# Performance work log

Hardware: AMD Instinct MI355X
Metric: run time of the kernel (lower is better)

## Reference

```python
import jax, jax.numpy as jnp
import numpy as np

DIM = 384
NUM_HEADS = 8


def setup_inputs() -> dict:
    key = jax.random.key(0)
    k1, k2, k3, k4 = jax.random.split(key, 4)
    B, N, D = 8, 16384, DIM
    x = jax.random.normal(k1, (B, N, D), dtype=jnp.float32)
    # nn.Linear(dim, 3*dim, bias=False): weight [3D, D]; store transposed [D, 3D]
    W_qkv = jax.random.normal(k2, (D, 3 * D), dtype=jnp.float32) * (1.0 / np.sqrt(D))
    W_proj = jax.random.normal(k3, (D, D), dtype=jnp.float32) * (1.0 / np.sqrt(D))
    b_proj = jax.random.normal(k4, (D,), dtype=jnp.float32) * 0.01
    return {"x": x, "W_qkv": W_qkv, "W_proj": W_proj, "b_proj": b_proj}


def reference(x, W_qkv, W_proj, b_proj):
    B, N, D = x.shape
    H = NUM_HEADS
    C = D // H
    # qkv: [B, N, 3, H, C] -> split; layout matches '(qkv H C)' packing
    qkv = (x @ W_qkv).reshape(B, N, 3, H, C)
    qkv = jnp.transpose(qkv, (2, 0, 3, 1, 4))  # [3, B, H, N, C]
    q = jax.nn.softmax(qkv[0], axis=-1)        # softmax over channel dim C
    k = jax.nn.softmax(qkv[1], axis=2)         # softmax over token dim N (== B H C N softmax last)
    v = qkv[2]
    # context = k^T @ v : [B, H, C, C] — tiny, avoids NxN scores
    context = jnp.einsum('bhnc,bhnd->bhcd', k, v)
    out = jnp.einsum('bhnc,bhcd->bhnd', q, context)  # [B, H, N, C]
    out = jnp.transpose(out, (0, 2, 1, 3)).reshape(B, N, D)  # 'B H N C -> B N (H C)'
    return out @ W_proj + b_proj
```

## Files before the change

kernel.cpp:

```cpp
#include <hip/hip_runtime.h>
#include <math.h>

#define B_ 8
#define N_ 16384
#define D_ 384
#define TD_ 1152
#define M_ (B_*N_)
#define CTX_ELEMS (B_*8*48*48)
#define Z_ELEMS   (B_*8*48)

typedef __attribute__((ext_vector_type(8))) short short8;
typedef __attribute__((ext_vector_type(4))) float f32x4;
typedef __attribute__((ext_vector_type(4))) unsigned short us4;
typedef __attribute__((ext_vector_type(8))) unsigned short us8;

__device__ __forceinline__ unsigned short f2bf(float f){
    union { float f; unsigned u; } v; v.f = f;
    unsigned r = v.u + 0x7FFFu + ((v.u >> 16) & 1u);
    return (unsigned short)(r >> 16);
}

#define MFMA(a,b,c) __builtin_amdgcn_mfma_f32_16x16x32_bf16((a),(b),(c),0,0,0)

__global__ void kP(const float* __restrict__ Wqkv, const float* __restrict__ Wp,
                   unsigned short* __restrict__ WqkvT, unsigned short* __restrict__ WpT)
{
    __shared__ float t[32][33];
    int bi = blockIdx.x;
    const float* src; unsigned short* dst; int ldS, c0, d0;
    if (bi < 432) { src = Wqkv; dst = WqkvT; ldS = 1152; c0 = (bi % 36) * 32; d0 = (bi / 36) * 32; }
    else { bi -= 432; src = Wp; dst = WpT; ldS = 384; c0 = (bi % 12) * 32; d0 = (bi / 12) * 32; }
    const int cx = threadIdx.x & 31, ry = threadIdx.x >> 5;
#pragma unroll
    for (int k = 0; k < 4; ++k) {
        int r = ry + k * 8;
        t[r][cx] = src[(size_t)(d0 + r) * ldS + c0 + cx];
    }
    __syncthreads();
#pragma unroll
    for (int k = 0; k < 4; ++k) {
        int r = ry + k * 8;
        dst[(size_t)(c0 + r) * 384 + d0 + cx] = f2bf(t[cx][r]);
    }
}

__global__ __launch_bounds__(512, 2) void kA(const float* __restrict__ x,
        const unsigned short* __restrict__ WqkvT,
        float* __restrict__ ctx, float* __restrict__ Z)
{
    __shared__ __align__(16) unsigned short xs[64 * 392];
    __shared__ __align__(16) unsigned short kv[8 * 96 * 64];

    const int tid = threadIdx.x;
    const int w   = tid >> 6;
    const int l   = tid & 63;
    const int q   = l >> 4;
    const int c16 = l & 15;
    const int blk = blockIdx.x;
    const int b   = blk >> 5;
    const int tbase = (blk & 31) * 8;
    unsigned short* kvw = kv + w * (96 * 64);

    f32x4 ctxacc[3][3];
    float zp[3] = {0.f, 0.f, 0.f};
#pragma unroll
    for (int i = 0; i < 3; ++i)
#pragma unroll
        for (int j = 0; j < 3; ++j) ctxacc[i][j] = (f32x4){0.f, 0.f, 0.f, 0.f};

    const int st = tid >> 3, sq = tid & 7;

    for (int g = 0; g < 8; ++g) {
        const size_t tok0 = (size_t)b * 16384 + (size_t)(tbase + g) * 64;
        __syncthreads();
        {
            const float* xg = x + (tok0 + st) * 384 + sq * 4;
            unsigned short* xw = xs + st * 392 + sq * 4;
#pragma unroll
            for (int i = 0; i < 12; ++i) {
                float4 v = *(const float4*)(xg + i * 32);
                us4 o; o.x = f2bf(v.x); o.y = f2bf(v.y); o.z = f2bf(v.z); o.w = f2bf(v.w);
                *(us4*)(xw + i * 32) = o;
            }
        }
        __syncthreads();

        f32x4 kva[4][6];
#pragma unroll
        for (int mt = 0; mt < 4; ++mt)
#pragma unroll
            for (int j = 0; j < 6; ++j) kva[mt][j] = (f32x4){0.f, 0.f, 0.f, 0.f};

#pragma unroll
        for (int ks = 0; ks < 12; ++ks) {
            short8 a[4];
#pragma unroll
            for (int mt = 0; mt < 4; ++mt)
                a[mt] = *(const short8*)(xs + (mt * 16 + c16) * 392 + ks * 32 + q * 8);
#pragma unroll
            for (int j = 0; j < 6; ++j) {
                const int colrow = (j < 3) ? (384 + w * 48 + j * 16 + c16)
                                           : (768 + w * 48 + (j - 3) * 16 + c16);
                short8 bf = *(const short8*)(WqkvT + (size_t)colrow * 384 + ks * 32 + q * 8);
#pragma unroll
                for (int mt = 0; mt < 4; ++mt)
                    kva[mt][j] = MFMA(a[mt], bf, kva[mt][j]);
            }
        }

#pragma unroll
        for (int mt = 0; mt < 4; ++mt) {
            const int chunk = 2 * mt + (q >> 1);
            const int tin = (q & 1) * 4;
#pragma unroll
            for (int j = 0; j < 6; ++j) {
                f32x4 vv = kva[mt][j];
                us4 o;
                int row;
                if (j < 3) {
                    row = j * 16 + c16;
                    float e0 = __expf(vv.x), e1 = __expf(vv.y), e2 = __expf(vv.z), e3 = __expf(vv.w);
                    zp[j] += (e0 + e1) + (e2 + e3);
                    o.x = f2bf(e0); o.y = f2bf(e1); o.z = f2bf(e2); o.w = f2bf(e3);
                } else {
                    row = 48 + (j - 3) * 16 + c16;
                    o.x = f2bf(vv.x); o.y = f2bf(vv.y); o.z = f2bf(vv.z); o.w = f2bf(vv.w);
                }
                *(us4*)(kvw + row * 64 + ((chunk ^ (row & 7)) << 3) + tin) = o;
            }
        }
        __syncthreads();

#pragma unroll
        for (int kt = 0; kt < 2; ++kt) {
            short8 af[3], bf2[3];
#pragma unroll
            for (int i = 0; i < 3; ++i) {
                const int ra = i * 16 + c16;
                af[i]  = *(const short8*)(kvw + ra * 64 + (((kt * 4 + q) ^ (ra & 7)) << 3));
                const int rb = 48 + i * 16 + c16;
                bf2[i] = *(const short8*)(kvw + rb * 64 + (((kt * 4 + q) ^ (rb & 7)) << 3));
            }
#pragma unroll
            for (int ct = 0; ct < 3; ++ct)
#pragma unroll
                for (int dt = 0; dt < 3; ++dt)
                    ctxacc[ct][dt] = MFMA(af[ct], bf2[dt], ctxacc[ct][dt]);
        }
    }

#pragma unroll
    for (int j = 0; j < 3; ++j) {
        float v = zp[j];
        v += __shfl_xor(v, 16);
        v += __shfl_xor(v, 32);
        if (l < 16) atomicAdd(&Z[(b * 8 + w) * 48 + j * 16 + c16], v);
    }
#pragma unroll
    for (int ct = 0; ct < 3; ++ct)
#pragma unroll
        for (int dt = 0; dt < 3; ++dt)
#pragma unroll
            for (int r = 0; r < 4; ++r) {
                const int c = ct * 16 + q * 4 + r;
                const int d = dt * 16 + c16;
                atomicAdd(&ctx[((size_t)(b * 8 + w) * 48 + c) * 48 + d], ctxacc[ct][dt][r]);
            }
}

__global__ void kB(const float* __restrict__ ctx, const float* __restrict__ Z,
                   unsigned short* __restrict__ ctxT)
{
    const int e = blockIdx.x * 256 + threadIdx.x;
    const int bh = e / 3072;
    const int r = e % 3072;
    const int d = r >> 6;
    const int c = r & 63;
    float v = 0.f;
    if (c < 48) v = ctx[((size_t)bh * 48 + c) * 48 + d] / Z[bh * 48 + c];
    ctxT[e] = f2bf(v);
}

__global__ __launch_bounds__(256, 2) void kC(const float* __restrict__ x,
        const unsigned short* __restrict__ WqkvT,
        const unsigned short* __restrict__ ctxT,
        const unsigned short* __restrict__ WpT,
        const float* __restrict__ bp, float* __restrict__ out)
{
    __shared__ __align__(16) unsigned short xs[32 * 392];
    __shared__ __align__(16) unsigned short qs[32 * 520];

    const int tid = threadIdx.x;
    const int w   = tid >> 6;
    const int l   = tid & 63;
    const int q   = l >> 4;
    const int c16 = l & 15;
    const int blk = blockIdx.x;
    const size_t tok0 = (size_t)blk * 32;
    const int b = blk >> 9;

    {
        const int st = tid >> 3, sq = tid & 7;
        const float* xg = x + (tok0 + st) * 384 + sq * 4;
        unsigned short* xw = xs + st * 392 + sq * 4;
#pragma unroll
        for (int i = 0; i < 12; ++i) {
            float4 v = *(const float4*)(xg + i * 32);
            us4 o; o.x = f2bf(v.x); o.y = f2bf(v.y); o.z = f2bf(v.z); o.w = f2bf(v.w);
            *(us4*)(xw + i * 32) = o;
        }
    }
    __syncthreads();

    f32x4 acc[2][6];
#pragma unroll
    for (int mt = 0; mt < 2; ++mt)
#pragma unroll
        for (int j = 0; j < 6; ++j) acc[mt][j] = (f32x4){0.f, 0.f, 0.f, 0.f};

#pragma unroll
    for (int ks = 0; ks < 12; ++ks) {
        short8 a0 = *(const short8*)(xs + (c16) * 392 + ks * 32 + q * 8);
        short8 a1 = *(const short8*)(xs + (16 + c16) * 392 + ks * 32 + q * 8);
#pragma unroll
        for (int j = 0; j < 6; ++j) {
            const int nt = w * 6 + j;
            short8 bf = *(const short8*)(WqkvT + (size_t)(nt * 16 + c16) * 384 + ks * 32 + q * 8);
            acc[0][j] = MFMA(a0, bf, acc[0][j]);
            acc[1][j] = MFMA(a1, bf, acc[1][j]);
        }
    }
    __syncthreads();

#pragma unroll
    for (int hh = 0; hh < 2; ++hh) {
        const int h = 2 * w + hh;
        f32x4 e[2][3];
#pragma unroll
        for (int mt = 0; mt < 2; ++mt)
#pragma unroll
            for (int jj = 0; jj < 3; ++jj) {
                f32x4 vv = acc[mt][hh * 3 + jj];
                e[mt][jj].x = __expf(vv.x); e[mt][jj].y = __expf(vv.y);
                e[mt][jj].z = __expf(vv.z); e[mt][jj].w = __expf(vv.w);
            }
#pragma unroll
        for (int mt = 0; mt < 2; ++mt)
#pragma unroll
            for (int r = 0; r < 4; ++r) {
                float s = e[mt][0][r] + e[mt][1][r] + e[mt][2][r];
                s += __shfl_xor(s, 1); s += __shfl_xor(s, 2);
                s += __shfl_xor(s, 4); s += __shfl_xor(s, 8);
                const float inv = 1.0f / s;
                e[mt][0][r] *= inv; e[mt][1][r] *= inv; e[mt][2][r] *= inv;
            }
#pragma unroll
        for (int mt = 0; mt < 2; ++mt)
#pragma unroll
            for (int jj = 0; jj < 3; ++jj) {
                const int c = jj * 16 + c16;
#pragma unroll
                for (int r = 0; r < 4; ++r) {
                    const int t = mt * 16 + q * 4 + r;
                    qs[t * 520 + h * 64 + c] = f2bf(e[mt][jj][r]);
                }
            }
    }
    {
        const int t = l & 31, hp = l >> 5;
        const int h = 2 * w + hp;
        us8 z8 = {0, 0, 0, 0, 0, 0, 0, 0};
        *(us8*)(qs + t * 520 + h * 64 + 48) = z8;
    }
    __syncthreads();

#pragma unroll
    for (int hh = 0; hh < 2; ++hh) {
        const int h = 2 * w + hh;
        f32x4 y[2][3];
#pragma unroll
        for (int mt = 0; mt < 2; ++mt)
#pragma unroll
            for (int dt = 0; dt < 3; ++dt) y[mt][dt] = (f32x4){0.f, 0.f, 0.f, 0.f};
#pragma unroll
        for (int ks = 0; ks < 2; ++ks) {
            short8 a0 = *(const short8*)(qs + (c16) * 520 + h * 64 + ks * 32 + q * 8);
            short8 a1 = *(const short8*)(qs + (16 + c16) * 520 + h * 64 + ks * 32 + q * 8);
#pragma unroll
            for (int dt = 0; dt < 3; ++dt) {
                short8 bf = *(const short8*)(ctxT + ((size_t)(b * 8 + h) * 48 + dt * 16 + c16) * 64 + ks * 32 + q * 8);
                y[0][dt] = MFMA(a0, bf, y[0][dt]);
                y[1][dt] = MFMA(a1, bf, y[1][dt]);
            }
        }
#pragma unroll
        for (int mt = 0; mt < 2; ++mt)
#pragma unroll
            for (int dt = 0; dt < 3; ++dt) {
                const int dcol = h * 48 + dt * 16 + c16;
#pragma unroll
                for (int r = 0; r < 4; ++r) {
                    const int t = mt * 16 + q * 4 + r;
                    xs[t * 392 + dcol] = f2bf(y[mt][dt][r]);
                }
            }
    }
    __syncthreads();

    f32x4 po[2][6];
#pragma unroll
    for (int mt = 0; mt < 2; ++mt)
#pragma unroll
        for (int j = 0; j < 6; ++j) po[mt][j] = (f32x4){0.f, 0.f, 0.f, 0.f};

#pragma unroll
    for (int ks = 0; ks < 12; ++ks) {
        short8 a0 = *(const short8*)(xs + (c16) * 392 + ks * 32 + q * 8);
        short8 a1 = *(const short8*)(xs + (16 + c16) * 392 + ks * 32 + q * 8);
#pragma unroll
        for (int j = 0; j < 6; ++j) {
            const int nt = w * 6 + j;
            short8 bf = *(const short8*)(WpT + (size_t)(nt * 16 + c16) * 384 + ks * 32 + q * 8);
            po[0][j] = MFMA(a0, bf, po[0][j]);
            po[1][j] = MFMA(a1, bf, po[1][j]);
        }
    }

#pragma unroll
    for (int j = 0; j < 6; ++j) {
        const int col = (w * 6 + j) * 16 + c16;
        const float bv = bp[col];
#pragma unroll
        for (int mt = 0; mt < 2; ++mt)
#pragma unroll
            for (int r = 0; r < 4; ++r) {
                const int t = mt * 16 + q * 4 + r;
                out[(tok0 + t) * 384 + col] = po[mt][j][r] + bv;
            }
    }
}

extern "C" void kernel_launch(void* const* d_in, const int* in_sizes, int n_in,
                              void* d_out, int out_size, void* d_ws, size_t ws_size,
                              hipStream_t stream)
{
    (void)in_sizes; (void)n_in; (void)out_size; (void)ws_size;
    const float* x    = (const float*)d_in[0];
    const float* Wqkv = (const float*)d_in[1];
    const float* Wp   = (const float*)d_in[2];
    const float* bp   = (const float*)d_in[3];
    float* out = (float*)d_out;

    char* p = (char*)d_ws;
    float* ctx = (float*)p;                 p += CTX_ELEMS * 4;
    float* Z   = (float*)p;                 p += Z_ELEMS * 4;
    unsigned short* WqkvT = (unsigned short*)p;  p += TD_ * D_ * 2;
    unsigned short* WpT   = (unsigned short*)p;  p += D_ * D_ * 2;
    unsigned short* ctxT  = (unsigned short*)p;

    hipMemsetAsync(d_ws, 0, (CTX_ELEMS + Z_ELEMS) * sizeof(float), stream);
    kP<<<dim3(576), dim3(256), 0, stream>>>(Wqkv, Wp, WqkvT, WpT);
    kA<<<dim3(256), dim3(512), 0, stream>>>(x, WqkvT, ctx, Z);
    kB<<<dim3(768), dim3(256), 0, stream>>>(ctx, Z, ctxT);
    kC<<<dim3(4096), dim3(256), 0, stream>>>(x, WqkvT, ctxT, WpT, bp, out);
}
```

Baseline: 824.8 us.

## Shrink kA token tile to 32 and double grid; per-wave q buffer in kC

kA now processes 32-token tiles instead of 64, computing the K and V halves sequentially to cut accumulator registers and LDS, with launch bounds raised to 4 blocks and the grid doubled to 512 blocks. This is meant to raise occupancy and spread the work over more CUs, at the cost of more global atomics on ctx and Z and more repeated weight loads. kC gives each wave its own small q staging buffer so the q@ctx product follows softmax directly, without a block-wide barrier. Its launch bounds are raised to 3 blocks per CU.

```diff
diff --git a/kernel.cpp b/kernel.cpp
--- a/kernel.cpp
+++ b/kernel.cpp
@@ -44,12 +44,12 @@
     }
 }
 
-__global__ __launch_bounds__(512, 2) void kA(const float* __restrict__ x,
+__global__ __launch_bounds__(512, 4) void kA(const float* __restrict__ x,
         const unsigned short* __restrict__ WqkvT,
         float* __restrict__ ctx, float* __restrict__ Z)
 {
-    __shared__ __align__(16) unsigned short xs[64 * 392];
-    __shared__ __align__(16) unsigned short kv[8 * 96 * 64];
+    __shared__ __align__(16) unsigned short xs[32 * 392];
+    __shared__ __align__(16) unsigned short kv[8 * 96 * 32];
 
     const int tid = threadIdx.x;
     const int w   = tid >> 6;
@@ -57,9 +57,9 @@
     const int q   = l >> 4;
     const int c16 = l & 15;
     const int blk = blockIdx.x;
-    const int b   = blk >> 5;
-    const int tbase = (blk & 31) * 8;
-    unsigned short* kvw = kv + w * (96 * 64);
+    const int b   = blk >> 6;
+    const int tile0 = (blk & 63) * 8;
+    unsigned short* kvw = kv + w * (96 * 32);
 
     f32x4 ctxacc[3][3];
     float zp[3] = {0.f, 0.f, 0.f};
@@ -68,85 +68,78 @@
 #pragma unroll
         for (int j = 0; j < 3; ++j) ctxacc[i][j] = (f32x4){0.f, 0.f, 0.f, 0.f};
 
-    const int st = tid >> 3, sq = tid & 7;
+    const int st = tid >> 4, sq = tid & 15;
 
     for (int g = 0; g < 8; ++g) {
-        const size_t tok0 = (size_t)b * 16384 + (size_t)(tbase + g) * 64;
+        const size_t tok0 = (size_t)b * 16384 + (size_t)(tile0 + g) * 32;
         __syncthreads();
         {
             const float* xg = x + (tok0 + st) * 384 + sq * 4;
             unsigned short* xw = xs + st * 392 + sq * 4;
 #pragma unroll
-            for (int i = 0; i < 12; ++i) {
-                float4 v = *(const float4*)(xg + i * 32);
+            for (int i = 0; i < 6; ++i) {
+                float4 v = *(const float4*)(xg + i * 64);
                 us4 o; o.x = f2bf(v.x); o.y = f2bf(v.y); o.z = f2bf(v.z); o.w = f2bf(v.w);
-                *(us4*)(xw + i * 32) = o;
+                *(us4*)(xw + i * 64) = o;
             }
         }
         __syncthreads();
 
-        f32x4 kva[4][6];
-#pragma unroll
-        for (int mt = 0; mt < 4; ++mt)
-#pragma unroll
-            for (int j = 0; j < 6; ++j) kva[mt][j] = (f32x4){0.f, 0.f, 0.f, 0.f};
-
-#pragma unroll
-        for (int ks = 0; ks < 12; ++ks) {
-            short8 a[4];
-#pragma unroll
-            for (int mt = 0; mt < 4; ++mt)
-                a[mt] = *(const short8*)(xs + (mt * 16 + c16) * 392 + ks * 32 + q * 8);
-#pragma unroll
-            for (int j = 0; j < 6; ++j) {
-                const int colrow = (j < 3) ? (384 + w * 48 + j * 16 + c16)
-                                           : (768 + w * 48 + (j - 3) * 16 + c16);
-                short8 bf = *(const short8*)(WqkvT + (size_t)colrow * 384 + ks * 32 + q * 8);
-#pragma unroll
-                for (int mt = 0; mt < 4; ++mt)
-                    kva[mt][j] = MFMA(a[mt], bf, kva[mt][j]);
-            }
-        }
-
-#pragma unroll
-        for (int mt = 0; mt < 4; ++mt) {
-            const int chunk = 2 * mt + (q >> 1);
-            const int tin = (q & 1) * 4;
-#pragma unroll
-            for (int j = 0; j < 6; ++j) {
-                f32x4 vv = kva[mt][j];
-                us4 o;
-                int row;
-                if (j < 3) {
-                    row = j * 16 + c16;
-                    float e0 = __expf(vv.x), e1 = __expf(vv.y), e2 = __expf(vv.z), e3 = __expf(vv.w);
-                    zp[j] += (e0 + e1) + (e2 + e3);
-                    o.x = f2bf(e0); o.y = f2bf(e1); o.z = f2bf(e2); o.w = f2bf(e3);
-                } else {
-                    row = 48 + (j - 3) * 16 + c16;
-                    o.x = f2bf(vv.x); o.y = f2bf(vv.y); o.z = f2bf(vv.z); o.w = f2bf(vv.w);
+#pragma unroll
+        for (int half = 0; half < 2; ++half) {
+            f32x4 acc2[2][3];
+#pragma unroll
+            for (int mt = 0; mt < 2; ++mt)
+#pragma unroll
+                for (int j = 0; j < 3; ++j) acc2[mt][j] = (f32x4){0.f, 0.f, 0.f, 0.f};
+
+#pragma unroll
+            for (int ks = 0; ks < 12; ++ks) {
+                short8 a0 = *(const short8*)(xs + (c16) * 392 + ks * 32 + q * 8);
+                short8 a1 = *(const short8*)(xs + (16 + c16) * 392 + ks * 32 + q * 8);
+#pragma unroll
+                for (int j = 0; j < 3; ++j) {
+                    const int col = 384 + half * 384 + w * 48 + j * 16 + c16;
+                    short8 bf = *(const short8*)(WqkvT + (size_t)col * 384 + ks * 32 + q * 8);
+                    acc2[0][j] = MFMA(a0, bf, acc2[0][j]);
+                    acc2[1][j] = MFMA(a1, bf, acc2[1][j]);
                 }
-                *(us4*)(kvw + row * 64 + ((chunk ^ (row & 7)) << 3) + tin) = o;
-            }
-        }
-        __syncthreads();
-
-#pragma unroll
-        for (int kt = 0; kt < 2; ++kt) {
-            short8 af[3], bf2[3];
-#pragma unroll
-            for (int i = 0; i < 3; ++i) {
-                const int ra = i * 16 + c16;
-                af[i]  = *(const short8*)(kvw + ra * 64 + (((kt * 4 + q) ^ (ra & 7)) << 3));
-                const int rb = 48 + i * 16 + c16;
-                bf2[i] = *(const short8*)(kvw + rb * 64 + (((kt * 4 + q) ^ (rb & 7)) << 3));
-            }
-#pragma unroll
-            for (int ct = 0; ct < 3; ++ct)
-#pragma unroll
-                for (int dt = 0; dt < 3; ++dt)
-                    ctxacc[ct][dt] = MFMA(af[ct], bf2[dt], ctxacc[ct][dt]);
-        }
+            }
+
+#pragma unroll
+            for (int mt = 0; mt < 2; ++mt) {
+                const int t8  = mt * 2 + (q >> 1);
+                const int tin = (q & 1) * 4;
+#pragma unroll
+                for (int j = 0; j < 3; ++j) {
+                    f32x4 vv = acc2[mt][j];
+                    const int row = half * 48 + j * 16 + c16;
+                    us4 o;
+                    if (half == 0) {
+                        float e0 = __expf(vv.x), e1 = __expf(vv.y), e2 = __expf(vv.z), e3 = __expf(vv.w);
+                        zp[j] += (e0 + e1) + (e2 + e3);
+                        o.x = f2bf(e0); o.y = f2bf(e1); o.z = f2bf(e2); o.w = f2bf(e3);
+                    } else {
+                        o.x = f2bf(vv.x); o.y = f2bf(vv.y); o.z = f2bf(vv.z); o.w = f2bf(vv.w);
+                    }
+                    *(us4*)(kvw + row * 32 + (((t8 ^ (row & 3))) << 3) + tin) = o;
+                }
+            }
+        }
+
+        short8 af[3], bf2[3];
+#pragma unroll
+        for (int i = 0; i < 3; ++i) {
+            const int ra = i * 16 + c16;
+            af[i]  = *(const short8*)(kvw + ra * 32 + ((q ^ (ra & 3)) << 3));
+            const int rb = 48 + i * 16 + c16;
+            bf2[i] = *(const short8*)(kvw + rb * 32 + ((q ^ (rb & 3)) << 3));
+        }
+#pragma unroll
+        for (int ct = 0; ct < 3; ++ct)
+#pragma unroll
+            for (int dt = 0; dt < 3; ++dt)
+                ctxacc[ct][dt] = MFMA(af[ct], bf2[dt], ctxacc[ct][dt]);
     }
 
 #pragma unroll
@@ -181,14 +174,14 @@
     ctxT[e] = f2bf(v);
 }
 
-__global__ __launch_bounds__(256, 2) void kC(const float* __restrict__ x,
+__global__ __launch_bounds__(256, 3) void kC(const float* __restrict__ x,
         const unsigned short* __restrict__ WqkvT,
         const unsigned short* __restrict__ ctxT,
         const unsigned short* __restrict__ WpT,
         const float* __restrict__ bp, float* __restrict__ out)
 {
     __shared__ __align__(16) unsigned short xs[32 * 392];
-    __shared__ __align__(16) unsigned short qs[32 * 520];
+    __shared__ __align__(16) unsigned short qs[4 * 32 * 72];
 
     const int tid = threadIdx.x;
     const int w   = tid >> 6;
@@ -198,6 +191,7 @@
     const int blk = blockIdx.x;
     const size_t tok0 = (size_t)blk * 32;
     const int b = blk >> 9;
+    unsigned short* qsw = qs + w * (32 * 72);
 
     {
         const int st = tid >> 3, sq = tid & 7;
@@ -231,6 +225,12 @@
         }
     }
     __syncthreads();
+
+    {
+        const int t = l & 31, p = l >> 5;
+        us8 z8 = {0, 0, 0, 0, 0, 0, 0, 0};
+        *(us8*)(qsw + t * 72 + 48 + p * 8) = z8;
+    }
 
 #pragma unroll
     for (int hh = 0; hh < 2; ++hh) {
@@ -262,21 +262,10 @@
 #pragma unroll
                 for (int r = 0; r < 4; ++r) {
                     const int t = mt * 16 + q * 4 + r;
-                    qs[t * 520 + h * 64 + c] = f2bf(e[mt][jj][r]);
+                    qsw[t * 72 + c] = f2bf(e[mt][jj][r]);
                 }
             }
-    }
-    {
-        const int t = l & 31, hp = l >> 5;
-        const int h = 2 * w + hp;
-        us8 z8 = {0, 0, 0, 0, 0, 0, 0, 0};
-        *(us8*)(qs + t * 520 + h * 64 + 48) = z8;
-    }
-    __syncthreads();
-
-#pragma unroll
-    for (int hh = 0; hh < 2; ++hh) {
-        const int h = 2 * w + hh;
+
         f32x4 y[2][3];
 #pragma unroll
         for (int mt = 0; mt < 2; ++mt)
@@ -284,8 +273,8 @@
             for (int dt = 0; dt < 3; ++dt) y[mt][dt] = (f32x4){0.f, 0.f, 0.f, 0.f};
 #pragma unroll
         for (int ks = 0; ks < 2; ++ks) {
-            short8 a0 = *(const short8*)(qs + (c16) * 520 + h * 64 + ks * 32 + q * 8);
-            short8 a1 = *(const short8*)(qs + (16 + c16) * 520 + h * 64 + ks * 32 + q * 8);
+            short8 a0 = *(const short8*)(qsw + (c16) * 72 + ks * 32 + q * 8);
+            short8 a1 = *(const short8*)(qsw + (16 + c16) * 72 + ks * 32 + q * 8);
 #pragma unroll
             for (int dt = 0; dt < 3; ++dt) {
                 short8 bf = *(const short8*)(ctxT + ((size_t)(b * 8 + h) * 48 + dt * 16 + c16) * 64 + ks * 32 + q * 8);
@@ -360,7 +349,7 @@
 
     hipMemsetAsync(d_ws, 0, (CTX_ELEMS + Z_ELEMS) * sizeof(float), stream);
     kP<<<dim3(576), dim3(256), 0, stream>>>(Wqkv, Wp, WqkvT, WpT);
-    kA<<<dim3(256), dim3(512), 0, stream>>>(x, WqkvT, ctx, Z);
+    kA<<<dim3(512), dim3(512), 0, stream>>>(x, WqkvT, ctx, Z);
     kB<<<dim3(768), dim3(256), 0, stream>>>(ctx, Z, ctxT);
     kC<<<dim3(4096), dim3(256), 0, stream>>>(x, WqkvT, ctxT, WpT, bp, out);
 }
```

Result: slower. 1.151 ms (+39.6%).
